# Kernel tuning notes

Measured on AMD Instinct MI355X. Metric: run time of the kernel, lower is better.

Reference implementation:

```python
import jax, jax.numpy as jnp
import numpy as np

D_STATE = 16


def setup_inputs() -> dict:
    key = jax.random.key(0)
    ks = jax.random.split(key, 7)
    B, S, D = 8, 4096, 64
    ds = D_STATE
    x = jax.random.normal(ks[0], (B, S, D), dtype=jnp.float32)
    # Selection layers modeled as Linear(d_model, out). W_A scaled small so the
    # random transition matrices are contractive over 4096 steps.
    W_A = jax.random.normal(ks[1], (D, ds * ds), dtype=jnp.float32) * 0.01
    b_A = jnp.zeros((ds * ds,), dtype=jnp.float32)
    W_B = jax.random.normal(ks[2], (D, ds * D), dtype=jnp.float32) * 0.05
    b_B = jnp.zeros((ds * D,), dtype=jnp.float32)
    W_C = jax.random.normal(ks[3], (D, ds * D), dtype=jnp.float32) * 0.05
    b_C = jnp.zeros((ds * D,), dtype=jnp.float32)
    return {"x": x, "W_A": W_A, "b_A": b_A, "W_B": W_B, "b_B": b_B,
            "W_C": W_C, "b_C": b_C}


def reference(x, W_A, b_A, W_B, b_B, W_C, b_C):
    B, S, D = x.shape
    ds = D_STATE
    # Input-dependent (selective) parameters per timestep
    A = (x @ W_A + b_A).reshape(B, S, ds, ds)      # [B,S,ds,ds]
    Bm = (x @ W_B + b_B).reshape(B, S, ds, D)      # [B,S,ds,D]
    Cm = (x @ W_C + b_C).reshape(B, S, ds, D)      # [B,S,ds,D]
    # Pre-contract B_t @ x_t once: [B,S,ds]
    Bx = jnp.einsum('bsnd,bsd->bsn', Bm, x)

    def step(h, inputs):
        A_t, Bx_t = inputs                          # [B,ds,ds], [B,ds]
        h = jnp.einsum('bij,bj->bi', A_t, h) + Bx_t
        return h, h

    h0 = jnp.zeros((B, ds), dtype=x.dtype)
    _, hs = jax.lax.scan(step, h0,
                         (jnp.swapaxes(A, 0, 1), jnp.swapaxes(Bx, 0, 1)))
    hs = jnp.swapaxes(hs, 0, 1)                     # [B,S,ds]
    # output_t = C_t^T @ h_t  -> [B,S,D]
    return jnp.einsum('bsnd,bsn->bsd', Cm, hs)
```

## Files before the change

### kernel.cpp

```cpp
#include <hip/hip_runtime.h>

#define BATCH   8
#define SEQ     4096
#define DM      64
#define DS      16
#define BS      (BATCH*SEQ)
#define CHUNK   16
#define NCHT    (BS/CHUNK)
#define SG      16
#define NSG     (NCHT/SG)

typedef __attribute__((ext_vector_type(8))) __bf16 bf16x8;
typedef __attribute__((ext_vector_type(4))) float  f32x4;

__device__ __forceinline__ unsigned short f2bf(float f) {
  unsigned int u = __float_as_uint(f);
  u += 0x7fffu + ((u >> 16) & 1u);
  return (unsigned short)(u >> 16);
}
__device__ __forceinline__ float bflo(unsigned int u) { return __uint_as_float(u << 16); }
__device__ __forceinline__ float bfhi(unsigned int u) { return __uint_as_float(u & 0xffff0000u); }

#define AS_I 20
#define AS_T 324

__global__ __launch_bounds__(256) void k0_castw(
    const float* __restrict__ WA, const float* __restrict__ WB,
    const float* __restrict__ WC,
    unsigned short* __restrict__ WAt, unsigned short* __restrict__ WBt,
    unsigned short* __restrict__ WCt)
{
  const int o = blockIdx.x * 256 + threadIdx.x;
  if (o < 16384) {
    const int c = o >> 6, e = o & 63;
    WAt[o] = f2bf(WA[e * 256 + c]);
  } else if (o < 16384 + 65536) {
    const int p = o - 16384;
    const int c = p >> 6, e = p & 63;
    WBt[p] = f2bf(WB[e * 1024 + c]);
  } else {
    const int p = o - 16384 - 65536;
    const int c = p >> 6, e = p & 63;
    WCt[p] = f2bf(WC[e * 1024 + c]);
  }
}

struct WFrag {
  bf16x8 b00, b01, b10, b11, b20, b21, b30, b31;
  bf16x8 a0f, a1f;
  float  ba;
};

__device__ __forceinline__ WFrag loadw(
    const unsigned short* __restrict__ WBt, const unsigned short* __restrict__ WAt,
    const float* __restrict__ bA, int n, int l15, int quad)
{
  WFrag f;
  const bf16x8* w0 = (const bf16x8*)(WBt + (size_t)((n * 4 + 0) * 16 + l15) * 64);
  const bf16x8* w1 = (const bf16x8*)(WBt + (size_t)((n * 4 + 1) * 16 + l15) * 64);
  const bf16x8* w2 = (const bf16x8*)(WBt + (size_t)((n * 4 + 2) * 16 + l15) * 64);
  const bf16x8* w3 = (const bf16x8*)(WBt + (size_t)((n * 4 + 3) * 16 + l15) * 64);
  f.b00 = w0[quad]; f.b01 = w0[quad + 4];
  f.b10 = w1[quad]; f.b11 = w1[quad + 4];
  f.b20 = w2[quad]; f.b21 = w2[quad + 4];
  f.b30 = w3[quad]; f.b31 = w3[quad + 4];
  const bf16x8* wa = (const bf16x8*)(WAt + (size_t)(n * 16 + l15) * 64);
  f.a0f = wa[quad]; f.a1f = wa[quad + 4];
  f.ba  = bA[n * 16 + l15];
  return f;
}

__global__ __launch_bounds__(256, 2) void g1(
    const float* __restrict__ x, const unsigned short* __restrict__ WBt,
    const float* __restrict__ bB, const unsigned short* __restrict__ WAt,
    const float* __restrict__ bA, unsigned short* __restrict__ xb,
    unsigned short* __restrict__ Wt_ws, float* __restrict__ u_ws,
    float* __restrict__ P_ws, float* __restrict__ v_ws)
{
  __shared__ __align__(16) float xs[64][68];
  __shared__ __align__(16) float bBs[1024];
  __shared__ __align__(16) unsigned short As[64 * AS_T];
  __shared__ __align__(16) float bxs[64][16];
  __shared__ __align__(16) float us[4][16];

  const int tid  = threadIdx.x;
  const int lane = tid & 63;
  const int l15  = lane & 15;
  const int quad = lane >> 4;
  const int w    = tid >> 6;
  const int t0   = blockIdx.x * 64;
  const int twl  = w * 16;

  {
    const float4* xg = (const float4*)(x + (size_t)t0 * DM);
    #pragma unroll
    for (int i = 0; i < 4; ++i) {
      const int f4 = tid + 256 * i;
      ((float4*)&xs[f4 >> 4][0])[f4 & 15] = xg[f4];
    }
    ((float4*)bBs)[tid] = ((const float4*)bB)[tid];
    if (tid < 64) us[tid >> 4][tid & 15] = 0.f;
  }
  __syncthreads();

  WFrag cur = loadw(WBt, WAt, bA, 0, l15, quad);

  bf16x8 a0, a1;
  {
    const int row = twl + l15;
    union { bf16x8 v; ushort4 s[2]; } ua, ub;
    float4 p0 = *(const float4*)&xs[row][quad * 8];
    float4 p1 = *(const float4*)&xs[row][quad * 8 + 4];
    float4 p2 = *(const float4*)&xs[row][32 + quad * 8];
    float4 p3 = *(const float4*)&xs[row][32 + quad * 8 + 4];
    ua.s[0] = (ushort4){f2bf(p0.x), f2bf(p0.y), f2bf(p0.z), f2bf(p0.w)};
    ua.s[1] = (ushort4){f2bf(p1.x), f2bf(p1.y), f2bf(p1.z), f2bf(p1.w)};
    ub.s[0] = (ushort4){f2bf(p2.x), f2bf(p2.y), f2bf(p2.z), f2bf(p2.w)};
    ub.s[1] = (ushort4){f2bf(p3.x), f2bf(p3.y), f2bf(p3.z), f2bf(p3.w)};
    a0 = ua.v; a1 = ub.v;
    unsigned short* xp = xb + (size_t)(t0 + row) * 64 + quad * 8;
    *(bf16x8*)xp        = a0;
    *(bf16x8*)(xp + 32) = a1;
  }

  float xv[4][4];
  #pragma unroll
  for (int r = 0; r < 4; ++r)
    #pragma unroll
    for (int reg = 0; reg < 4; ++reg)
      xv[r][reg] = xs[twl + quad * 4 + reg][r * 16 + l15];

  #pragma unroll
  for (int n = 0; n < 16; ++n) {
    WFrag nxt = (n < 15) ? loadw(WBt, WAt, bA, n + 1, l15, quad) : cur;

    const f32x4 z4 = {0.f, 0.f, 0.f, 0.f};
    f32x4 aac = z4;
    aac = __builtin_amdgcn_mfma_f32_16x16x32_bf16(a0, cur.a0f, aac, 0, 0, 0);
    aac = __builtin_amdgcn_mfma_f32_16x16x32_bf16(a1, cur.a1f, aac, 0, 0, 0);

    f32x4 ac0 = z4, ac1 = z4, ac2 = z4, ac3 = z4;
    ac0 = __builtin_amdgcn_mfma_f32_16x16x32_bf16(a0, cur.b00, ac0, 0, 0, 0);
    ac0 = __builtin_amdgcn_mfma_f32_16x16x32_bf16(a1, cur.b01, ac0, 0, 0, 0);
    ac1 = __builtin_amdgcn_mfma_f32_16x16x32_bf16(a0, cur.b10, ac1, 0, 0, 0);
    ac1 = __builtin_amdgcn_mfma_f32_16x16x32_bf16(a1, cur.b11, ac1, 0, 0, 0);
    ac2 = __builtin_amdgcn_mfma_f32_16x16x32_bf16(a0, cur.b20, ac2, 0, 0, 0);
    ac2 = __builtin_amdgcn_mfma_f32_16x16x32_bf16(a1, cur.b21, ac2, 0, 0, 0);
    ac3 = __builtin_amdgcn_mfma_f32_16x16x32_bf16(a0, cur.b30, ac3, 0, 0, 0);
    ac3 = __builtin_amdgcn_mfma_f32_16x16x32_bf16(a1, cur.b31, ac3, 0, 0, 0);

    const float bb0 = bBs[n * 64 +  0 + l15];
    const float bb1 = bBs[n * 64 + 16 + l15];
    const float bb2 = bBs[n * 64 + 32 + l15];
    const float bb3 = bBs[n * 64 + 48 + l15];
    float part[4];
    #pragma unroll
    for (int reg = 0; reg < 4; ++reg) {
      float s = fmaf(ac0[reg] + bb0, xv[0][reg], 0.f);
      s = fmaf(ac1[reg] + bb1, xv[1][reg], s);
      s = fmaf(ac2[reg] + bb2, xv[2][reg], s);
      s = fmaf(ac3[reg] + bb3, xv[3][reg], s);
      part[reg] = s;
    }
    #pragma unroll
    for (int off = 1; off < 16; off <<= 1) {
      #pragma unroll
      for (int reg = 0; reg < 4; ++reg)
        part[reg] += __shfl_xor(part[reg], off, 64);
    }
    if (l15 == 0) {
      #pragma unroll
      for (int reg = 0; reg < 4; ++reg)
        bxs[twl + quad * 4 + reg][n] = part[reg];
    }

    As[(twl + quad * 4 + 0) * AS_T + n * AS_I + l15] = f2bf(aac[0] + cur.ba);
    As[(twl + quad * 4 + 1) * AS_T + n * AS_I + l15] = f2bf(aac[1] + cur.ba);
    As[(twl + quad * 4 + 2) * AS_T + n * AS_I + l15] = f2bf(aac[2] + cur.ba);
    As[(twl + quad * 4 + 3) * AS_T + n * AS_I + l15] = f2bf(aac[3] + cur.ba);

    cur = nxt;
  }

  {
    bf16x8 wb;
    #pragma unroll
    for (int j = 0; j < 8; ++j) wb[j] = (__bf16)((quad * 8 + j == l15) ? 1.f : 0.f);
    f32x4 d = {0.f, 0.f, 0.f, 0.f};
    const int qq = quad & 1;

    const unsigned short* rpp = &As[twl * AS_T + l15 * AS_I];
    uint2 r0 = *(const uint2*)(rpp);
    uint2 r1 = *(const uint2*)(rpp + 4);
    uint2 r2 = *(const uint2*)(rpp + 8);
    uint2 r3 = *(const uint2*)(rpp + 12);

    #pragma unroll 1
    for (int t = 0; t < CHUNK; ++t) {
      const int tl = twl + t;

      uint2 s0, s1, s2, s3;
      if (t < CHUNK - 1) {
        const unsigned short* rp = &As[(tl + 1) * AS_T + l15 * AS_I];
        s0 = *(const uint2*)(rp);
        s1 = *(const uint2*)(rp + 4);
        s2 = *(const uint2*)(rp + 8);
        s3 = *(const uint2*)(rp + 12);
      } else { s0 = r0; s1 = r1; s2 = r2; s3 = r3; }

      uint4 abits;
      if (quad == 0)      abits = make_uint4(r0.x, r0.y, r1.x, r1.y);
      else if (quad == 1) abits = make_uint4(r2.x, r2.y, r3.x, r3.y);
      else                abits = make_uint4(0u, 0u, 0u, 0u);
      bf16x8 af = *(bf16x8*)&abits;

      f32x4 z4 = {0.f, 0.f, 0.f, 0.f};
      d = __builtin_amdgcn_mfma_f32_16x16x32_bf16(af, wb, z4, 0, 0, 0);

      float nu;
      {
        float4 U0 = *(const float4*)&us[w][0];
        float4 U1 = *(const float4*)&us[w][4];
        float4 U2 = *(const float4*)&us[w][8];
        float4 U3 = *(const float4*)&us[w][12];
        float n0 = bxs[tl][l15], n1 = 0.f, n2 = 0.f, n3 = 0.f;
        n0 = fmaf(bflo(r0.x), U0.x, n0); n0 = fmaf(bfhi(r0.x), U0.y, n0);
        n0 = fmaf(bflo(r0.y), U0.z, n0); n0 = fmaf(bfhi(r0.y), U0.w, n0);
        n1 = fmaf(bflo(r1.x), U1.x, n1); n1 = fmaf(bfhi(r1.x), U1.y, n1);
        n1 = fmaf(bflo(r1.y), U1.z, n1); n1 = fmaf(bfhi(r1.y), U1.w, n1);
        n2 = fmaf(bflo(r2.x), U2.x, n2); n2 = fmaf(bfhi(r2.x), U2.y, n2);
        n2 = fmaf(bflo(r2.y), U2.z, n2); n2 = fmaf(bfhi(r2.y), U2.w, n2);
        n3 = fmaf(bflo(r3.x), U3.x, n3); n3 = fmaf(bfhi(r3.x), U3.y, n3);
        n3 = fmaf(bflo(r3.y), U3.z, n3); n3 = fmaf(bfhi(r3.y), U3.w, n3);
        nu = (n0 + n1) + (n2 + n3);
      }

      bf16x8 nb;
      nb[0] = (__bf16)__shfl(d[0], (2 * qq + 0) * 16 + l15, 64);
      nb[1] = (__bf16)__shfl(d[1], (2 * qq + 0) * 16 + l15, 64);
      nb[2] = (__bf16)__shfl(d[2], (2 * qq + 0) * 16 + l15, 64);
      nb[3] = (__bf16)__shfl(d[3], (2 * qq + 0) * 16 + l15, 64);
      nb[4] = (__bf16)__shfl(d[0], (2 * qq + 1) * 16 + l15, 64);
      nb[5] = (__bf16)__shfl(d[1], (2 * qq + 1) * 16 + l15, 64);
      nb[6] = (__bf16)__shfl(d[2], (2 * qq + 1) * 16 + l15, 64);
      nb[7] = (__bf16)__shfl(d[3], (2 * qq + 1) * 16 + l15, 64);
      wb = nb;

      if (quad == 0) {
        us[w][l15] = nu;
        bxs[tl][l15] = nu;
      }
      #pragma unroll
      for (int r = 0; r < 4; ++r)
        As[tl * AS_T + (quad * 4 + r) * AS_I + l15] = f2bf(d[r]);

      r0 = s0; r1 = s1; r2 = s2; r3 = s3;
    }

    const int chunk = blockIdx.x * 4 + w;
    #pragma unroll
    for (int r = 0; r < 4; ++r)
      P_ws[(size_t)chunk * 256 + (quad * 4 + r) * 16 + l15] = d[r];
    if (quad == 0) v_ws[(size_t)chunk * DS + l15] = us[w][l15];
  }
  __syncthreads();

  {
    uint4* Wg = (uint4*)(Wt_ws + (size_t)t0 * 256);
    #pragma unroll 1
    for (int z = 0; z < 8; ++z) {
      const int p4 = z * 256 + tid;
      const int f  = p4 * 8;
      const int t  = f >> 8, i = (f >> 4) & 15, k = f & 15;
      const unsigned short* sp = &As[t * AS_T + i * AS_I + k];
      uint2 lo = *(const uint2*)(sp);
      uint2 hi = *(const uint2*)(sp + 4);
      Wg[p4] = make_uint4(lo.x, lo.y, hi.x, hi.y);
    }
    ((float4*)(u_ws + (size_t)t0 * DS))[tid] = ((const float4*)&bxs[0][0])[tid];
  }
}

__global__ __launch_bounds__(256, 1) void k3a(
    const float* __restrict__ P_ws, const float* __restrict__ v_ws,
    float* __restrict__ Q_ws, float* __restrict__ w_ws)
{
  __shared__ float wsv[4][16];
  const int tid  = threadIdx.x;
  const int lane = tid & 63;
  const int l15  = lane & 15;
  const int quad = lane >> 4;
  const int wv   = tid >> 6;
  const int s    = blockIdx.x * 4 + wv;
  const int qq   = quad & 1;

  if (lane < 16) wsv[wv][lane] = 0.f;
  bf16x8 wb;
  #pragma unroll
  for (int j = 0; j < 8; ++j) wb[j] = (__bf16)((quad * 8 + j == l15) ? 1.f : 0.f);
  f32x4 d = {0.f, 0.f, 0.f, 0.f};

  float4 p0 = {0.f,0.f,0.f,0.f}, p1 = {0.f,0.f,0.f,0.f};
  float nv;
  {
    const int chunk = s * SG;
    if (quad < 2) {
      const float4* pr = (const float4*)(P_ws + (size_t)chunk * 256 + l15 * 16 + quad * 8);
      p0 = pr[0]; p1 = pr[1];
    }
    nv = v_ws[(size_t)chunk * DS + l15];
  }

  #pragma unroll 1
  for (int t = 0; t < SG; ++t) {
    float4 q0 = {0.f,0.f,0.f,0.f}, q1 = {0.f,0.f,0.f,0.f};
    float nv2 = 0.f;
    if (t < SG - 1) {
      const int chunk = s * SG + t + 1;
      if (quad < 2) {
        const float4* pr = (const float4*)(P_ws + (size_t)chunk * 256 + l15 * 16 + quad * 8);
        q0 = pr[0]; q1 = pr[1];
      }
      nv2 = v_ws[(size_t)chunk * DS + l15];
    }

    bf16x8 af;
    af[0] = (__bf16)p0.x; af[1] = (__bf16)p0.y; af[2] = (__bf16)p0.z; af[3] = (__bf16)p0.w;
    af[4] = (__bf16)p1.x; af[5] = (__bf16)p1.y; af[6] = (__bf16)p1.z; af[7] = (__bf16)p1.w;

    f32x4 z4 = {0.f, 0.f, 0.f, 0.f};
    d = __builtin_amdgcn_mfma_f32_16x16x32_bf16(af, wb, z4, 0, 0, 0);

    float part = 0.f;
    if (quad < 2) {
      const float* wrow = &wsv[wv][quad * 8];
      part = p0.x*wrow[0] + p0.y*wrow[1] + p0.z*wrow[2] + p0.w*wrow[3]
           + p1.x*wrow[4] + p1.y*wrow[5] + p1.z*wrow[6] + p1.w*wrow[7];
    }
    part += __shfl_xor(part, 16, 64);

    bf16x8 nb;
    nb[0] = (__bf16)__shfl(d[0], (2 * qq + 0) * 16 + l15, 64);
    nb[1] = (__bf16)__shfl(d[1], (2 * qq + 0) * 16 + l15, 64);
    nb[2] = (__bf16)__shfl(d[2], (2 * qq + 0) * 16 + l15, 64);
    nb[3] = (__bf16)__shfl(d[3], (2 * qq + 0) * 16 + l15, 64);
    nb[4] = (__bf16)__shfl(d[0], (2 * qq + 1) * 16 + l15, 64);
    nb[5] = (__bf16)__shfl(d[1], (2 * qq + 1) * 16 + l15, 64);
    nb[6] = (__bf16)__shfl(d[2], (2 * qq + 1) * 16 + l15, 64);
    nb[7] = (__bf16)__shfl(d[3], (2 * qq + 1) * 16 + l15, 64);
    wb = nb;

    if (quad == 0) wsv[wv][l15] = part + nv;

    p0 = q0; p1 = q1; nv = nv2;
  }

  #pragma unroll
  for (int r = 0; r < 4; ++r)
    Q_ws[(size_t)s * 256 + (quad * 4 + r) * 16 + l15] = d[r];
  if (quad == 0) w_ws[(size_t)s * DS + l15] = wsv[wv][l15];
}

__global__ __launch_bounds__(128, 1) void k3b(
    const float* __restrict__ Q_ws, const float* __restrict__ w_ws,
    float* __restrict__ hbg_ws)
{
  const int tid = threadIdx.x;
  const int b = tid >> 4;
  const int r = tid & 15;
  float h = 0.f;

  float4 c0, c1, c2, c3; float vc;
  {
    const int s = b * 16;
    const float4* Pr = (const float4*)&Q_ws[(size_t)s * 256 + r * 16];
    c0 = Pr[0]; c1 = Pr[1]; c2 = Pr[2]; c3 = Pr[3];
    vc = w_ws[(size_t)s * DS + r];
  }

  #pragma unroll 1
  for (int g = 0; g < 16; ++g) {
    const int s = b * 16 + g;
    float4 d0, d1, d2, d3; float vc2;
    if (g < 15) {
      const float4* Pr = (const float4*)&Q_ws[(size_t)(s + 1) * 256 + r * 16];
      d0 = Pr[0]; d1 = Pr[1]; d2 = Pr[2]; d3 = Pr[3];
      vc2 = w_ws[(size_t)(s + 1) * DS + r];
    } else { d0 = c0; d1 = c1; d2 = c2; d3 = c3; vc2 = vc; }

    hbg_ws[(size_t)s * DS + r] = h;
    float a0 = c0.x*__shfl(h, 0,16) + c0.y*__shfl(h, 1,16) + c0.z*__shfl(h, 2,16) + c0.w*__shfl(h, 3,16);
    float a1 = c1.x*__shfl(h, 4,16) + c1.y*__shfl(h, 5,16) + c1.z*__shfl(h, 6,16) + c1.w*__shfl(h, 7,16);
    float a2 = c2.x*__shfl(h, 8,16) + c2.y*__shfl(h, 9,16) + c2.z*__shfl(h,10,16) + c2.w*__shfl(h,11,16);
    float a3 = c3.x*__shfl(h,12,16) + c3.y*__shfl(h,13,16) + c3.z*__shfl(h,14,16) + c3.w*__shfl(h,15,16);
    h = vc + ((a0 + a1) + (a2 + a3));

    c0 = d0; c1 = d1; c2 = d2; c3 = d3; vc = vc2;
  }
}

__global__ __launch_bounds__(256, 1) void k3c(
    const float* __restrict__ P_ws, const float* __restrict__ v_ws,
    const float* __restrict__ hbg_ws, float* __restrict__ hb_ws)
{
  const int tid = threadIdx.x;
  const int s = blockIdx.x * 16 + (tid >> 4);
  const int r = tid & 15;
  float h = hbg_ws[(size_t)s * DS + r];

  float4 c0, c1, c2, c3; float vc;
  {
    const int chunk = s * SG;
    const float4* Pr = (const float4*)&P_ws[(size_t)chunk * 256 + r * 16];
    c0 = Pr[0]; c1 = Pr[1]; c2 = Pr[2]; c3 = Pr[3];
    vc = v_ws[(size_t)chunk * DS + r];
  }

  #pragma unroll 1
  for (int t = 0; t < SG; ++t) {
    const int chunk = s * SG + t;
    float4 d0, d1, d2, d3; float vc2;
    if (t < SG - 1) {
      const float4* Pr = (const float4*)&P_ws[(size_t)(chunk + 1) * 256 + r * 16];
      d0 = Pr[0]; d1 = Pr[1]; d2 = Pr[2]; d3 = Pr[3];
      vc2 = v_ws[(size_t)(chunk + 1) * DS + r];
    } else { d0 = c0; d1 = c1; d2 = c2; d3 = c3; vc2 = vc; }

    hb_ws[(size_t)chunk * DS + r] = h;
    float a0 = c0.x*__shfl(h, 0,16) + c0.y*__shfl(h, 1,16) + c0.z*__shfl(h, 2,16) + c0.w*__shfl(h, 3,16);
    float a1 = c1.x*__shfl(h, 4,16) + c1.y*__shfl(h, 5,16) + c1.z*__shfl(h, 6,16) + c1.w*__shfl(h, 7,16);
    float a2 = c2.x*__shfl(h, 8,16) + c2.y*__shfl(h, 9,16) + c2.z*__shfl(h,10,16) + c2.w*__shfl(h,11,16);
    float a3 = c3.x*__shfl(h,12,16) + c3.y*__shfl(h,13,16) + c3.z*__shfl(h,14,16) + c3.w*__shfl(h,15,16);
    h = vc + ((a0 + a1) + (a2 + a3));

    c0 = d0; c1 = d1; c2 = d2; c3 = d3; vc = vc2;
  }
}

struct CFrag2 {
  bf16x8 c00, c01, c10, c11;
};

__device__ __forceinline__ CFrag2 loadc2(
    const unsigned short* __restrict__ WCt, int n, int r0c, int r1c, int l15, int quad)
{
  CFrag2 f;
  const bf16x8* w0 = (const bf16x8*)(WCt + (size_t)((n * 4 + r0c) * 16 + l15) * 64);
  const bf16x8* w1 = (const bf16x8*)(WCt + (size_t)((n * 4 + r1c) * 16 + l15) * 64);
  f.c00 = w0[quad]; f.c01 = w0[quad + 4];
  f.c10 = w1[quad]; f.c11 = w1[quad + 4];
  return f;
}

__global__ __launch_bounds__(256, 4) void g2(
    const unsigned short* __restrict__ xb, const unsigned short* __restrict__ WCt,
    const float* __restrict__ bC, const unsigned short* __restrict__ Wt_ws,
    const float* __restrict__ u_ws, const float* __restrict__ hb_ws,
    float* __restrict__ out)
{
  __shared__ float hsh[32][17];
  __shared__ float bCs[1024];
  const int tid  = threadIdx.x;
  const int lane = tid & 63;
  const int l15  = lane & 15;
  const int quad = lane >> 4;
  const int w    = tid >> 6;
  const int tg   = w >> 1;
  const int dh   = w & 1;
  const int t0   = blockIdx.x * 32;
  const int twl  = tg * 16;
  const int r0c  = dh * 2 + 0;
  const int r1c  = dh * 2 + 1;

  ((float4*)bCs)[tid] = ((const float4*)bC)[tid];

  const bf16x8* xvp = (const bf16x8*)(xb + (size_t)(t0 + twl + l15) * 64);
  bf16x8 a0 = xvp[quad];
  bf16x8 a1 = xvp[quad + 4];

  #pragma unroll
  for (int z = 0; z < 2; ++z) {
    const int gcell = z * 256 + tid;
    const int tl = gcell >> 4, i = gcell & 15;
    const int t = t0 + tl;
    const uint4* wr = (const uint4*)(Wt_ws + (size_t)t * 256 + i * 16);
    uint4 wa = wr[0], wbv = wr[1];
    const float4* hp = (const float4*)(hb_ws + (size_t)(t >> 4) * DS);
    float4 h0 = hp[0], h1 = hp[1], h2 = hp[2], h3 = hp[3];
    float p0 = u_ws[(size_t)t * DS + i], p1 = 0.f, p2 = 0.f, p3 = 0.f;
    p0 = fmaf(bflo(wa.x),  h0.x, p0); p0 = fmaf(bfhi(wa.x),  h0.y, p0);
    p0 = fmaf(bflo(wa.y),  h0.z, p0); p0 = fmaf(bfhi(wa.y),  h0.w, p0);
    p1 = fmaf(bflo(wa.z),  h1.x, p1); p1 = fmaf(bfhi(wa.z),  h1.y, p1);
    p1 = fmaf(bflo(wa.w),  h1.z, p1); p1 = fmaf(bfhi(wa.w),  h1.w, p1);
    p2 = fmaf(bflo(wbv.x), h2.x, p2); p2 = fmaf(bfhi(wbv.x), h2.y, p2);
    p2 = fmaf(bflo(wbv.y), h2.z, p2); p2 = fmaf(bfhi(wbv.y), h2.w, p2);
    p3 = fmaf(bflo(wbv.z), h3.x, p3); p3 = fmaf(bfhi(wbv.z), h3.y, p3);
    p3 = fmaf(bflo(wbv.w), h3.z, p3); p3 = fmaf(bfhi(wbv.w), h3.w, p3);
    hsh[tl][i] = (p0 + p1) + (p2 + p3);
  }
  __syncthreads();

  f32x4 o0 = {0.f, 0.f, 0.f, 0.f}, o1 = {0.f, 0.f, 0.f, 0.f};

  CFrag2 cur = loadc2(WCt, 0, r0c, r1c, l15, quad);
  #pragma unroll
  for (int n = 0; n < 16; ++n) {
    CFrag2 nxt = (n < 15) ? loadc2(WCt, n + 1, r0c, r1c, l15, quad) : cur;

    const f32x4 z4 = {0.f, 0.f, 0.f, 0.f};
    f32x4 ac0 = z4, ac1 = z4;
    ac0 = __builtin_amdgcn_mfma_f32_16x16x32_bf16(a0, cur.c00, ac0, 0, 0, 0);
    ac0 = __builtin_amdgcn_mfma_f32_16x16x32_bf16(a1, cur.c01, ac0, 0, 0, 0);
    ac1 = __builtin_amdgcn_mfma_f32_16x16x32_bf16(a0, cur.c10, ac1, 0, 0, 0);
    ac1 = __builtin_amdgcn_mfma_f32_16x16x32_bf16(a1, cur.c11, ac1, 0, 0, 0);

    float hn[4];
    #pragma unroll
    for (int reg = 0; reg < 4; ++reg) hn[reg] = hsh[twl + quad * 4 + reg][n];

    const float bc0 = bCs[n * 64 + r0c * 16 + l15];
    const float bc1 = bCs[n * 64 + r1c * 16 + l15];
    #pragma unroll
    for (int reg = 0; reg < 4; ++reg) {
      o0[reg] = fmaf(ac0[reg] + bc0, hn[reg], o0[reg]);
      o1[reg] = fmaf(ac1[reg] + bc1, hn[reg], o1[reg]);
    }

    cur = nxt;
  }

  #pragma unroll
  for (int reg = 0; reg < 4; ++reg) {
    out[(size_t)(t0 + twl + quad * 4 + reg) * DM + r0c * 16 + l15] = o0[reg];
    out[(size_t)(t0 + twl + quad * 4 + reg) * DM + r1c * 16 + l15] = o1[reg];
  }
}

extern "C" void kernel_launch(void* const* d_in, const int* in_sizes, int n_in,
                              void* d_out, int out_size, void* d_ws, size_t ws_size,
                              hipStream_t stream) {
  const float* x  = (const float*)d_in[0];
  const float* WA = (const float*)d_in[1];
  const float* bA = (const float*)d_in[2];
  const float* WB = (const float*)d_in[3];
  const float* bB = (const float*)d_in[4];
  const float* WC = (const float*)d_in[5];
  const float* bC = (const float*)d_in[6];
  float* out = (float*)d_out;

  float* ws     = (float*)d_ws;
  float* P_ws   = ws;
  float* v_ws   = P_ws   + (size_t)NCHT * 256;
  float* u_ws   = v_ws   + (size_t)NCHT * DS;
  float* Q_ws   = u_ws   + (size_t)BS * DS;
  float* w_ws   = Q_ws   + (size_t)NSG * 256;
  float* hbg_ws = w_ws   + (size_t)NSG * DS;
  float* hb_ws  = hbg_ws + (size_t)NSG * DS;
  unsigned short* xb    = (unsigned short*)(hb_ws + (size_t)NCHT * DS);
  unsigned short* WAt   = xb  + (size_t)BS * 64;
  unsigned short* WBt   = WAt + 256 * 64;
  unsigned short* WCt   = WBt + 1024 * 64;
  unsigned short* Wt_ws = WCt + 1024 * 64;

  k0_castw<<<576,      256, 0, stream>>>(WA, WB, WC, WAt, WBt, WCt);
  g1      <<<BS / 64,  256, 0, stream>>>(x, WBt, bB, WAt, bA, xb, Wt_ws, u_ws, P_ws, v_ws);
  k3a     <<<NSG / 4,  256, 0, stream>>>(P_ws, v_ws, Q_ws, w_ws);
  k3b     <<<1,        128, 0, stream>>>(Q_ws, w_ws, hbg_ws);
  k3c     <<<NSG / 16, 256, 0, stream>>>(P_ws, v_ws, hbg_ws, hb_ws);
  g2      <<<BS / 32,  256, 0, stream>>>(xb, WCt, bC, Wt_ws, u_ws, hb_ws, out);
}
```

Before: 190.9 us.

## Fuse three scan stages into one per-batch kernel with L2 prefetch blocks

Merges the three-level chunked scan (chunk-group composition, cross-group carry, intra-group propagation) into a single kernel where each batch's 16 groups are handled by one 1024-thread block using shared memory for the group transitions and carries. This removes two kernel launches and the global round-trips of the Q/w/hbg intermediates. Extra blocks (index 8 and up) do nothing but load Wt_ws, xb and u_ws so those buffers are warm in cache for the following g2 kernel. The spare blocks add memory traffic, and each batch's scan is now serialized within one block.

```diff
diff --git a/kernel.cpp b/kernel.cpp
--- a/kernel.cpp
+++ b/kernel.cpp
@@ -281,159 +281,157 @@
   }
 }
 
-__global__ __launch_bounds__(256, 1) void k3a(
+__global__ __launch_bounds__(1024, 4) void k3f(
     const float* __restrict__ P_ws, const float* __restrict__ v_ws,
-    float* __restrict__ Q_ws, float* __restrict__ w_ws)
+    float* __restrict__ hb_ws,
+    const unsigned short* __restrict__ Wt_ws,
+    const unsigned short* __restrict__ xb,
+    const float* __restrict__ u_ws)
 {
-  __shared__ float wsv[4][16];
-  const int tid  = threadIdx.x;
+  __shared__ float Qs[16][256];
+  __shared__ float wsv[16][16];
+  __shared__ float hbgs[16][16];
+
+  const int tid = threadIdx.x;
+  const int bx  = blockIdx.x;
+
+  if (bx >= 8) {
+    const uint4* wp = (const uint4*)(Wt_ws + (size_t)bx * 32 * 256);
+    uint4 a = wp[tid];
+    const unsigned int* xp = (const unsigned int*)(xb + (size_t)bx * 32 * 64);
+    unsigned int b = xp[tid];
+    unsigned int c = 0;
+    if (tid < 512) c = ((const unsigned int*)(u_ws + (size_t)bx * 32 * DS))[tid];
+    asm volatile("" :: "v"(a.x), "v"(b), "v"(c));
+    return;
+  }
+
   const int lane = tid & 63;
   const int l15  = lane & 15;
   const int quad = lane >> 4;
   const int wv   = tid >> 6;
-  const int s    = blockIdx.x * 4 + wv;
   const int qq   = quad & 1;
 
-  if (lane < 16) wsv[wv][lane] = 0.f;
-  bf16x8 wb;
-  #pragma unroll
-  for (int j = 0; j < 8; ++j) wb[j] = (__bf16)((quad * 8 + j == l15) ? 1.f : 0.f);
-  f32x4 d = {0.f, 0.f, 0.f, 0.f};
-
-  float4 p0 = {0.f,0.f,0.f,0.f}, p1 = {0.f,0.f,0.f,0.f};
-  float nv;
   {
-    const int chunk = s * SG;
-    if (quad < 2) {
-      const float4* pr = (const float4*)(P_ws + (size_t)chunk * 256 + l15 * 16 + quad * 8);
-      p0 = pr[0]; p1 = pr[1];
-    }
-    nv = v_ws[(size_t)chunk * DS + l15];
-  }
-
-  #pragma unroll 1
-  for (int t = 0; t < SG; ++t) {
-    float4 q0 = {0.f,0.f,0.f,0.f}, q1 = {0.f,0.f,0.f,0.f};
-    float nv2 = 0.f;
-    if (t < SG - 1) {
-      const int chunk = s * SG + t + 1;
+    const int s = bx * 16 + wv;
+    if (lane < 16) wsv[wv][lane] = 0.f;
+    bf16x8 wb;
+    #pragma unroll
+    for (int j = 0; j < 8; ++j) wb[j] = (__bf16)((quad * 8 + j == l15) ? 1.f : 0.f);
+    f32x4 d = {0.f, 0.f, 0.f, 0.f};
+
+    float4 p0 = {0.f,0.f,0.f,0.f}, p1 = {0.f,0.f,0.f,0.f};
+    float nv;
+    {
+      const int chunk = s * SG;
       if (quad < 2) {
         const float4* pr = (const float4*)(P_ws + (size_t)chunk * 256 + l15 * 16 + quad * 8);
-        q0 = pr[0]; q1 = pr[1];
+        p0 = pr[0]; p1 = pr[1];
       }
-      nv2 = v_ws[(size_t)chunk * DS + l15];
-    }
-
-    bf16x8 af;
-    af[0] = (__bf16)p0.x; af[1] = (__bf16)p0.y; af[2] = (__bf16)p0.z; af[3] = (__bf16)p0.w;
-    af[4] = (__bf16)p1.x; af[5] = (__bf16)p1.y; af[6] = (__bf16)p1.z; af[7] = (__bf16)p1.w;
-
-    f32x4 z4 = {0.f, 0.f, 0.f, 0.f};
-    d = __builtin_amdgcn_mfma_f32_16x16x32_bf16(af, wb, z4, 0, 0, 0);
-
-    float part = 0.f;
-    if (quad < 2) {
-      const float* wrow = &wsv[wv][quad * 8];
-      part = p0.x*wrow[0] + p0.y*wrow[1] + p0.z*wrow[2] + p0.w*wrow[3]
-           + p1.x*wrow[4] + p1.y*wrow[5] + p1.z*wrow[6] + p1.w*wrow[7];
-    }
-    part += __shfl_xor(part, 16, 64);
-
-    bf16x8 nb;
-    nb[0] = (__bf16)__shfl(d[0], (2 * qq + 0) * 16 + l15, 64);
-    nb[1] = (__bf16)__shfl(d[1], (2 * qq + 0) * 16 + l15, 64);
-    nb[2] = (__bf16)__shfl(d[2], (2 * qq + 0) * 16 + l15, 64);
-    nb[3] = (__bf16)__shfl(d[3], (2 * qq + 0) * 16 + l15, 64);
-    nb[4] = (__bf16)__shfl(d[0], (2 * qq + 1) * 16 + l15, 64);
-    nb[5] = (__bf16)__shfl(d[1], (2 * qq + 1) * 16 + l15, 64);
-    nb[6] = (__bf16)__shfl(d[2], (2 * qq + 1) * 16 + l15, 64);
-    nb[7] = (__bf16)__shfl(d[3], (2 * qq + 1) * 16 + l15, 64);
-    wb = nb;
-
-    if (quad == 0) wsv[wv][l15] = part + nv;
-
-    p0 = q0; p1 = q1; nv = nv2;
-  }
-
-  #pragma unroll
-  for (int r = 0; r < 4; ++r)
-    Q_ws[(size_t)s * 256 + (quad * 4 + r) * 16 + l15] = d[r];
-  if (quad == 0) w_ws[(size_t)s * DS + l15] = wsv[wv][l15];
-}
-
-__global__ __launch_bounds__(128, 1) void k3b(
-    const float* __restrict__ Q_ws, const float* __restrict__ w_ws,
-    float* __restrict__ hbg_ws)
-{
-  const int tid = threadIdx.x;
-  const int b = tid >> 4;
-  const int r = tid & 15;
-  float h = 0.f;
-
-  float4 c0, c1, c2, c3; float vc;
-  {
-    const int s = b * 16;
-    const float4* Pr = (const float4*)&Q_ws[(size_t)s * 256 + r * 16];
-    c0 = Pr[0]; c1 = Pr[1]; c2 = Pr[2]; c3 = Pr[3];
-    vc = w_ws[(size_t)s * DS + r];
-  }
-
-  #pragma unroll 1
-  for (int g = 0; g < 16; ++g) {
-    const int s = b * 16 + g;
-    float4 d0, d1, d2, d3; float vc2;
-    if (g < 15) {
-      const float4* Pr = (const float4*)&Q_ws[(size_t)(s + 1) * 256 + r * 16];
-      d0 = Pr[0]; d1 = Pr[1]; d2 = Pr[2]; d3 = Pr[3];
-      vc2 = w_ws[(size_t)(s + 1) * DS + r];
-    } else { d0 = c0; d1 = c1; d2 = c2; d3 = c3; vc2 = vc; }
-
-    hbg_ws[(size_t)s * DS + r] = h;
-    float a0 = c0.x*__shfl(h, 0,16) + c0.y*__shfl(h, 1,16) + c0.z*__shfl(h, 2,16) + c0.w*__shfl(h, 3,16);
-    float a1 = c1.x*__shfl(h, 4,16) + c1.y*__shfl(h, 5,16) + c1.z*__shfl(h, 6,16) + c1.w*__shfl(h, 7,16);
-    float a2 = c2.x*__shfl(h, 8,16) + c2.y*__shfl(h, 9,16) + c2.z*__shfl(h,10,16) + c2.w*__shfl(h,11,16);
-    float a3 = c3.x*__shfl(h,12,16) + c3.y*__shfl(h,13,16) + c3.z*__shfl(h,14,16) + c3.w*__shfl(h,15,16);
-    h = vc + ((a0 + a1) + (a2 + a3));
-
-    c0 = d0; c1 = d1; c2 = d2; c3 = d3; vc = vc2;
-  }
-}
-
-__global__ __launch_bounds__(256, 1) void k3c(
-    const float* __restrict__ P_ws, const float* __restrict__ v_ws,
-    const float* __restrict__ hbg_ws, float* __restrict__ hb_ws)
-{
-  const int tid = threadIdx.x;
-  const int s = blockIdx.x * 16 + (tid >> 4);
-  const int r = tid & 15;
-  float h = hbg_ws[(size_t)s * DS + r];
-
-  float4 c0, c1, c2, c3; float vc;
-  {
-    const int chunk = s * SG;
-    const float4* Pr = (const float4*)&P_ws[(size_t)chunk * 256 + r * 16];
-    c0 = Pr[0]; c1 = Pr[1]; c2 = Pr[2]; c3 = Pr[3];
-    vc = v_ws[(size_t)chunk * DS + r];
-  }
-
-  #pragma unroll 1
-  for (int t = 0; t < SG; ++t) {
-    const int chunk = s * SG + t;
-    float4 d0, d1, d2, d3; float vc2;
-    if (t < SG - 1) {
-      const float4* Pr = (const float4*)&P_ws[(size_t)(chunk + 1) * 256 + r * 16];
-      d0 = Pr[0]; d1 = Pr[1]; d2 = Pr[2]; d3 = Pr[3];
-      vc2 = v_ws[(size_t)(chunk + 1) * DS + r];
-    } else { d0 = c0; d1 = c1; d2 = c2; d3 = c3; vc2 = vc; }
-
-    hb_ws[(size_t)chunk * DS + r] = h;
-    float a0 = c0.x*__shfl(h, 0,16) + c0.y*__shfl(h, 1,16) + c0.z*__shfl(h, 2,16) + c0.w*__shfl(h, 3,16);
-    float a1 = c1.x*__shfl(h, 4,16) + c1.y*__shfl(h, 5,16) + c1.z*__shfl(h, 6,16) + c1.w*__shfl(h, 7,16);
-    float a2 = c2.x*__shfl(h, 8,16) + c2.y*__shfl(h, 9,16) + c2.z*__shfl(h,10,16) + c2.w*__shfl(h,11,16);
-    float a3 = c3.x*__shfl(h,12,16) + c3.y*__shfl(h,13,16) + c3.z*__shfl(h,14,16) + c3.w*__shfl(h,15,16);
-    h = vc + ((a0 + a1) + (a2 + a3));
-
-    c0 = d0; c1 = d1; c2 = d2; c3 = d3; vc = vc2;
+      nv = v_ws[(size_t)chunk * DS + l15];
+    }
+
+    #pragma unroll 1
+    for (int t = 0; t < SG; ++t) {
+      float4 q0 = {0.f,0.f,0.f,0.f}, q1 = {0.f,0.f,0.f,0.f};
+      float nv2 = 0.f;
+      if (t < SG - 1) {
+        const int chunk = s * SG + t + 1;
+        if (quad < 2) {
+          const float4* pr = (const float4*)(P_ws + (size_t)chunk * 256 + l15 * 16 + quad * 8);
+          q0 = pr[0]; q1 = pr[1];
+        }
+        nv2 = v_ws[(size_t)chunk * DS + l15];
+      }
+
+      bf16x8 af;
+      af[0] = (__bf16)p0.x; af[1] = (__bf16)p0.y; af[2] = (__bf16)p0.z; af[3] = (__bf16)p0.w;
+      af[4] = (__bf16)p1.x; af[5] = (__bf16)p1.y; af[6] = (__bf16)p1.z; af[7] = (__bf16)p1.w;
+
+      f32x4 z4 = {0.f, 0.f, 0.f, 0.f};
+      d = __builtin_amdgcn_mfma_f32_16x16x32_bf16(af, wb, z4, 0, 0, 0);
+
+      float part = 0.f;
+      if (quad < 2) {
+        const float* wrow = &wsv[wv][quad * 8];
+        part = p0.x*wrow[0] + p0.y*wrow[1] + p0.z*wrow[2] + p0.w*wrow[3]
+             + p1.x*wrow[4] + p1.y*wrow[5] + p1.z*wrow[6] + p1.w*wrow[7];
+      }
+      part += __shfl_xor(part, 16, 64);
+
+      bf16x8 nb;
+      nb[0] = (__bf16)__shfl(d[0], (2 * qq + 0) * 16 + l15, 64);
+      nb[1] = (__bf16)__shfl(d[1], (2 * qq + 0) * 16 + l15, 64);
+      nb[2] = (__bf16)__shfl(d[2], (2 * qq + 0) * 16 + l15, 64);
+      nb[3] = (__bf16)__shfl(d[3], (2 * qq + 0) * 16 + l15, 64);
+      nb[4] = (__bf16)__shfl(d[0], (2 * qq + 1) * 16 + l15, 64);
+      nb[5] = (__bf16)__shfl(d[1], (2 * qq + 1) * 16 + l15, 64);
+      nb[6] = (__bf16)__shfl(d[2], (2 * qq + 1) * 16 + l15, 64);
+      nb[7] = (__bf16)__shfl(d[3], (2 * qq + 1) * 16 + l15, 64);
+      wb = nb;
+
+      if (quad == 0) wsv[wv][l15] = part + nv;
+
+      p0 = q0; p1 = q1; nv = nv2;
+    }
+
+    #pragma unroll
+    for (int r = 0; r < 4; ++r)
+      Qs[wv][(quad * 4 + r) * 16 + l15] = d[r];
+  }
+  __syncthreads();
+
+  if (tid < 16) {
+    const int r = tid;
+    float h = 0.f;
+    #pragma unroll 1
+    for (int g = 0; g < 16; ++g) {
+      hbgs[g][r] = h;
+      const float4* Pr = (const float4*)&Qs[g][r * 16];
+      float4 c0 = Pr[0], c1 = Pr[1], c2 = Pr[2], c3 = Pr[3];
+      const float vc = wsv[g][r];
+      float a0 = c0.x*__shfl(h, 0,16) + c0.y*__shfl(h, 1,16) + c0.z*__shfl(h, 2,16) + c0.w*__shfl(h, 3,16);
+      float a1 = c1.x*__shfl(h, 4,16) + c1.y*__shfl(h, 5,16) + c1.z*__shfl(h, 6,16) + c1.w*__shfl(h, 7,16);
+      float a2 = c2.x*__shfl(h, 8,16) + c2.y*__shfl(h, 9,16) + c2.z*__shfl(h,10,16) + c2.w*__shfl(h,11,16);
+      float a3 = c3.x*__shfl(h,12,16) + c3.y*__shfl(h,13,16) + c3.z*__shfl(h,14,16) + c3.w*__shfl(h,15,16);
+      h = vc + ((a0 + a1) + (a2 + a3));
+    }
+  }
+  __syncthreads();
+
+  if (tid < 256) {
+    const int g = tid >> 4;
+    const int r = tid & 15;
+    const int s = bx * 16 + g;
+    float h = hbgs[g][r];
+
+    float4 c0, c1, c2, c3; float vc;
+    {
+      const int chunk = s * SG;
+      const float4* Pr = (const float4*)&P_ws[(size_t)chunk * 256 + r * 16];
+      c0 = Pr[0]; c1 = Pr[1]; c2 = Pr[2]; c3 = Pr[3];
+      vc = v_ws[(size_t)chunk * DS + r];
+    }
+
+    #pragma unroll 1
+    for (int t = 0; t < SG; ++t) {
+      const int chunk = s * SG + t;
+      float4 d0, d1, d2, d3; float vc2;
+      if (t < SG - 1) {
+        const float4* Pr = (const float4*)&P_ws[(size_t)(chunk + 1) * 256 + r * 16];
+        d0 = Pr[0]; d1 = Pr[1]; d2 = Pr[2]; d3 = Pr[3];
+        vc2 = v_ws[(size_t)(chunk + 1) * DS + r];
+      } else { d0 = c0; d1 = c1; d2 = c2; d3 = c3; vc2 = vc; }
+
+      hb_ws[(size_t)chunk * DS + r] = h;
+      float a0 = c0.x*__shfl(h, 0,16) + c0.y*__shfl(h, 1,16) + c0.z*__shfl(h, 2,16) + c0.w*__shfl(h, 3,16);
+      float a1 = c1.x*__shfl(h, 4,16) + c1.y*__shfl(h, 5,16) + c1.z*__shfl(h, 6,16) + c1.w*__shfl(h, 7,16);
+      float a2 = c2.x*__shfl(h, 8,16) + c2.y*__shfl(h, 9,16) + c2.z*__shfl(h,10,16) + c2.w*__shfl(h,11,16);
+      float a3 = c3.x*__shfl(h,12,16) + c3.y*__shfl(h,13,16) + c3.z*__shfl(h,14,16) + c3.w*__shfl(h,15,16);
+      h = vc + ((a0 + a1) + (a2 + a3));
+
+      c0 = d0; c1 = d1; c2 = d2; c3 = d3; vc = vc2;
+    }
   }
 }
 
@@ -564,8 +562,6 @@
 
   k0_castw<<<576,      256, 0, stream>>>(WA, WB, WC, WAt, WBt, WCt);
   g1      <<<BS / 64,  256, 0, stream>>>(x, WBt, bB, WAt, bA, xb, Wt_ws, u_ws, P_ws, v_ws);
-  k3a     <<<NSG / 4,  256, 0, stream>>>(P_ws, v_ws, Q_ws, w_ws);
-  k3b     <<<1,        128, 0, stream>>>(Q_ws, w_ws, hbg_ws);
-  k3c     <<<NSG / 16, 256, 0, stream>>>(P_ws, v_ws, hbg_ws, hb_ws);
+  k3f     <<<1024,    1024, 0, stream>>>(P_ws, v_ws, hb_ws, Wt_ws, xb, u_ws);
   g2      <<<BS / 32,  256, 0, stream>>>(xb, WCt, bC, Wt_ws, u_ws, hb_ws, out);
 }
```

New measurement: 185.4 us. -2.8%, faster.
